# Kernel optimization log

Hardware: AMD Instinct MI355X
Metric: run time of the kernel (lower is better)

The kernel has to match this reference:

```python
import jax, jax.numpy as jnp
import numpy as np

B, CIN, COUT, K, H, W = 2, 128, 64, 64, 128, 128
BN_EPS = 1e-5


def setup_inputs() -> dict:
    key = jax.random.key(0)
    k1, k2, k3, k4 = jax.random.split(key, 4)
    x = jax.random.normal(k1, (B, CIN, H, W), dtype=jnp.float32)
    index = jax.random.randint(k2, (B, 1, H, W), 0, K)  # superpixel labels
    # kaiming_uniform(a=sqrt(5)) ~ uniform with bound sqrt(6/((1+5)*fan_in)) = 1/sqrt(fan_in)
    Wft = jax.random.uniform(k3, (CIN, COUT), dtype=jnp.float32,
                             minval=-1.0, maxval=1.0) / np.sqrt(CIN).astype(np.float32)
    Wm = jax.random.uniform(k4, (COUT, COUT), dtype=jnp.float32,
                            minval=-1.0, maxval=1.0) / np.sqrt(COUT).astype(np.float32)
    gamma = jnp.ones((COUT,), jnp.float32)
    beta = jnp.zeros((COUT,), jnp.float32)
    return {"x": x, "index": index, "Wft": Wft, "Wm": Wm, "gamma": gamma, "beta": beta}


def _gnn_forward(x, index, Wft, Wm, gamma, beta):
    # FeatureTransform: [B,Cin,H,W] -> [B,Cout,H,W]
    xt = jnp.einsum('bchw,co->bohw', x, Wft)

    idx = index[:, 0]                                   # [B,H,W]
    oh = jax.nn.one_hot(idx, K, dtype=xt.dtype)         # [B,H,W,K]

    # RegionalMeans (segment-mean over superpixels; equivalent to the
    # repeated-tensor multiply+sum in the torch code, without the 5D blowup)
    block_sum = oh.sum(axis=(1, 2))                     # [B,K]
    sums = jnp.einsum('bhwk,bohw->bko', oh, xt)         # [B,K,Cout]
    denom = block_sum + (block_sum == 0).astype(xt.dtype)
    means = sums / denom[..., None]                     # [B,K,Cout]

    # Adj: pairwise Mahalanobis distance with learned cov = Wm @ Wm.T
    cov = Wm @ Wm.T
    inv_cov = jnp.linalg.inv(cov)
    diff = means[:, :, None, :] - means[:, None, :, :]  # [B,K,K,Cout]
    q = jnp.einsum('bijc,cd,bijd->bij', diff, inv_cov, diff)
    dist = jnp.sqrt(jnp.maximum(q, 1e-12))              # clamp: diagonal q==0
    adj = jnp.exp(-dist)                                # [B,K,K]

    # GCN propagate: adjacency-weighted aggregation of region means
    adj_means = jnp.einsum('bij,bjo->bio', adj, means)  # [B,K,Cout]

    # sum_k one_hot_k * (x_rep + adj_means_k) == xt + gather(adj_means, idx)
    gathered = jnp.take_along_axis(adj_means, idx.reshape(B, -1, 1), axis=1)
    gathered = gathered.reshape(B, H, W, COUT).transpose(0, 3, 1, 2)
    features = jax.nn.relu(xt + gathered)               # [B,Cout,H,W]

    # BatchNorm2d (training-mode batch statistics, biased variance)
    mean = features.mean(axis=(0, 2, 3), keepdims=True)
    var = features.var(axis=(0, 2, 3), keepdims=True)
    out = (features - mean) / jnp.sqrt(var + BN_EPS)
    out = out * gamma[None, :, None, None] + beta[None, :, None, None]
    return out


def reference(x, index, Wft, Wm, gamma, beta):
    return _gnn_forward(x, index, Wft, Wm, gamma, beta)
```

## Files before the change

### kernel.cpp

```cpp
#include <hip/hip_runtime.h>
#include <hip/hip_bf16.h>

#define CIN   128
#define COUT  64
#define HW    16384
#define NB1   512

typedef __hip_bfloat16 bf16;

#define OFF_XT    0u
#define OFF_PS    2097152u
#define OFF_PC    3145728u
#define OFF_MEANS 3162112u
#define OFF_DIAG  3170304u
#define OFF_INV   3170432u
#define OFF_ADJM  3174528u
#define OFF_BNP   3182720u

__device__ __forceinline__ float rdlane(float v, int lane) {
  return __int_as_float(__builtin_amdgcn_readlane(__float_as_int(v), lane));
}

__global__ __launch_bounds__(256) void k1_xt_bins_inv(
    const float* __restrict__ x, const int* __restrict__ index,
    const float* __restrict__ Wft, const float* __restrict__ Wm,
    float* __restrict__ ws)
{
  __shared__ __align__(16) float smem[8704];
  const int blk = blockIdx.x, tid = threadIdx.x;
  if (blk < NB1) {
    float* lds_sums = smem;
    float* lds_cnt  = smem + 64 * 65;
    for (int i = tid; i < 64 * 65 + 64; i += 256) smem[i] = 0.f;
    __syncthreads();
    const int b    = blk >> 8;
    const int pg   = blk & 255;
    const int lane = tid & 63;
    const int og   = tid >> 6;
    const int o0   = __builtin_amdgcn_readfirstlane(og << 4);
    const int px   = (pg << 6) + lane;
    const float* xp = x + (size_t)b * CIN * HW + px;
    const int k = index[b * HW + px];
    float acc[16];
#pragma unroll
    for (int j = 0; j < 16; ++j) acc[j] = 0.f;
    float xa[8], xb[8];
#pragma unroll
    for (int u = 0; u < 8; ++u) xa[u] = xp[(size_t)u * HW];
    for (int cb = 0; cb < 128; cb += 8) {
      if (cb + 8 < 128) {
#pragma unroll
        for (int u = 0; u < 8; ++u) xb[u] = xp[(size_t)(cb + 8 + u) * HW];
      }
#pragma unroll
      for (int u = 0; u < 8; ++u) {
        const float xv = xa[u];
        const float4* w4 = (const float4*)(Wft + ((cb + u) << 6) + o0);
        const float4 w0 = w4[0], w1 = w4[1], w2 = w4[2], w3 = w4[3];
        acc[ 0]=fmaf(xv,w0.x,acc[ 0]); acc[ 1]=fmaf(xv,w0.y,acc[ 1]);
        acc[ 2]=fmaf(xv,w0.z,acc[ 2]); acc[ 3]=fmaf(xv,w0.w,acc[ 3]);
        acc[ 4]=fmaf(xv,w1.x,acc[ 4]); acc[ 5]=fmaf(xv,w1.y,acc[ 5]);
        acc[ 6]=fmaf(xv,w1.z,acc[ 6]); acc[ 7]=fmaf(xv,w1.w,acc[ 7]);
        acc[ 8]=fmaf(xv,w2.x,acc[ 8]); acc[ 9]=fmaf(xv,w2.y,acc[ 9]);
        acc[10]=fmaf(xv,w2.z,acc[10]); acc[11]=fmaf(xv,w2.w,acc[11]);
        acc[12]=fmaf(xv,w3.x,acc[12]); acc[13]=fmaf(xv,w3.y,acc[13]);
        acc[14]=fmaf(xv,w3.z,acc[14]); acc[15]=fmaf(xv,w3.w,acc[15]);
      }
#pragma unroll
      for (int u = 0; u < 8; ++u) xa[u] = xb[u];
    }
    float* xtp = ws + OFF_XT + (size_t)(b * COUT + o0) * HW + px;
#pragma unroll
    for (int j = 0; j < 16; ++j) xtp[(size_t)j * HW] = acc[j];
#pragma unroll
    for (int j = 0; j < 16; ++j) atomicAdd(&lds_sums[k * 65 + o0 + j], acc[j]);
    if (og == 0) atomicAdd(&lds_cnt[k], 1.f);
    __syncthreads();
    bf16* pb = (bf16*)(ws + OFF_PS) + (size_t)blk * 4096;
    for (int e = tid; e < 4096; e += 256)
      pb[e] = __float2bfloat16(lds_sums[(e >> 6) * 65 + (e & 63)]);
    if (tid < 64)
      ((bf16*)(ws + OFF_PC))[blk * 64 + tid] = __float2bfloat16(lds_cnt[tid]);
  } else {
    float* wm  = smem;
    float* cov = smem + 64 * 68;
    for (int e = tid; e < 4096; e += 256) wm[(e >> 6) * 68 + (e & 63)] = Wm[e];
    __syncthreads();
    {
      const int i0 = (tid >> 4) << 2, j0 = (tid & 15) << 2;
      float c4[16];
#pragma unroll
      for (int q = 0; q < 16; ++q) c4[q] = 0.f;
      for (int cq = 0; cq < 64; cq += 4) {
        float4 a[4], bb[4];
#pragma unroll
        for (int ii = 0; ii < 4; ++ii) a[ii]  = *(const float4*)&wm[(i0+ii)*68 + cq];
#pragma unroll
        for (int jj = 0; jj < 4; ++jj) bb[jj] = *(const float4*)&wm[(j0+jj)*68 + cq];
#pragma unroll
        for (int ii = 0; ii < 4; ++ii)
#pragma unroll
          for (int jj = 0; jj < 4; ++jj)
            c4[ii*4+jj] = fmaf(a[ii].x, bb[jj].x, fmaf(a[ii].y, bb[jj].y,
                          fmaf(a[ii].z, bb[jj].z, fmaf(a[ii].w, bb[jj].w, c4[ii*4+jj]))));
      }
#pragma unroll
      for (int ii = 0; ii < 4; ++ii)
#pragma unroll
        for (int jj = 0; jj < 4; ++jj)
          cov[(i0+ii)*68 + (j0+jj)] = c4[ii*4+jj];
    }
    __syncthreads();
    if (tid < 64) {
      float r[64];
#pragma unroll
      for (int j = 0; j < 64; ++j) r[j] = cov[tid * 68 + j];
#pragma unroll
      for (int k = 0; k < 64; ++k) {
        const float piv = rdlane(r[k], k);
        const float rp  = 1.0f / piv;
        const float a   = (tid == k) ? (rp - 1.0f) : (-r[k] * rp);
#pragma unroll
        for (int j = 0; j < 64; ++j) {
          const float s = rdlane(r[j], k);
          r[j] = fmaf(a, s, r[j]);
        }
        r[k] = (tid == k) ? rp : a;
      }
#pragma unroll
      for (int j = 0; j < 64; ++j) ws[OFF_INV + tid * 64 + j] = r[j];
    }
  }
}

__global__ __launch_bounds__(1024) void k15_means_diag(float* __restrict__ ws)
{
  __shared__ float red[16 * 64];
  __shared__ float lds_c[4];
  __shared__ float lds_m[64];
  const int blk = blockIdx.x, t = threadIdx.x;
  const int b = blk >> 6, k = blk & 63;
  const int o = t & 63, chunk = t >> 6;
  const bf16* ps = (const bf16*)(ws + OFF_PS);
  float s = 0.f;
#pragma unroll
  for (int s16 = 0; s16 < 16; ++s16) {
    const int i = chunk * 16 + s16;
    s += __bfloat162float(ps[(size_t)(b * 256 + i) * 4096 + (k << 6) + o]);
  }
  red[chunk * 64 + o] = s;
  float cv = 0.f;
  if (t < 256) cv = __bfloat162float(((const bf16*)(ws + OFF_PC))[(b * 256 + t) * 64 + k]);
#pragma unroll
  for (int m = 32; m; m >>= 1) cv += __shfl_xor(cv, m, 64);
  if (t < 256 && (t & 63) == 0) lds_c[t >> 6] = cv;
  __syncthreads();
  if (t < 64) {
    float m_raw = 0.f;
#pragma unroll
    for (int ch = 0; ch < 16; ++ch) m_raw += red[ch * 64 + o];
    const float cnt = lds_c[0] + lds_c[1] + lds_c[2] + lds_c[3];
    const float denom = cnt + ((cnt == 0.f) ? 1.f : 0.f);
    const float m = m_raw / denom;
    ws[OFF_MEANS + (size_t)(b * 64 + k) * 64 + o] = m;
    lds_m[o] = m;
    float inner = 0.f;
#pragma unroll 8
    for (int d = 0; d < 64; ++d) inner = fmaf(ws[OFF_INV + d * 64 + o], lds_m[d], inner);
    float p = m * inner;
#pragma unroll
    for (int mm = 32; mm; mm >>= 1) p += __shfl_xor(p, mm, 64);
    if (o == 0) ws[OFF_DIAG + b * 64 + k] = p;
  }
}

__global__ __launch_bounds__(256) void k2_adj(float* __restrict__ ws)
{
  __shared__ __align__(16) float means_s[64 * 68];
  __shared__ __align__(16) float inv_s[64 * 68];
  __shared__ __align__(16) float T_s[8 * 68];
  __shared__ __align__(16) float adj_s[8 * 68];
  __shared__ float diag_s[64];
  const int b = blockIdx.x >> 3;
  const int i0 = (blockIdx.x & 7) << 3;
  const int t = threadIdx.x;
  const float* mg = ws + OFF_MEANS + b * 4096;
  for (int e = t; e < 4096; e += 256) means_s[(e >> 6) * 68 + (e & 63)] = mg[e];
  const float* ig = ws + OFF_INV;
  for (int e = t; e < 4096; e += 256) inv_s[(e >> 6) * 68 + (e & 63)] = ig[e];
  if (t < 64) diag_s[t] = ws[OFF_DIAG + b * 64 + t];
  __syncthreads();
  if (t < 128) {
    const int i = t >> 4, d0 = (t & 15) << 2;
    float4 acc = {0.f, 0.f, 0.f, 0.f};
    for (int c = 0; c < 64; ++c) {
      const float mv = means_s[(i0 + i) * 68 + c];
      const float4 iv = *(const float4*)&inv_s[c * 68 + d0];
      acc.x = fmaf(mv, iv.x, acc.x); acc.y = fmaf(mv, iv.y, acc.y);
      acc.z = fmaf(mv, iv.z, acc.z); acc.w = fmaf(mv, iv.w, acc.w);
    }
    *(float4*)&T_s[i * 68 + d0] = acc;
  }
  __syncthreads();
  {
    const int i = t >> 5, jb = t & 31;
#pragma unroll
    for (int jj = 0; jj < 2; ++jj) {
      const int j = jb + (jj << 5);
      float4 p4 = {0.f, 0.f, 0.f, 0.f};
      for (int dq = 0; dq < 64; dq += 4) {
        const float4 tv = *(const float4*)&T_s[i * 68 + dq];
        const float4 mv = *(const float4*)&means_s[j * 68 + dq];
        p4.x = fmaf(tv.x, mv.x, p4.x); p4.y = fmaf(tv.y, mv.y, p4.y);
        p4.z = fmaf(tv.z, mv.z, p4.z); p4.w = fmaf(tv.w, mv.w, p4.w);
      }
      const float p = (p4.x + p4.y) + (p4.z + p4.w);
      const float q = diag_s[i0 + i] + diag_s[j] - 2.f * p;
      adj_s[i * 68 + j] = __expf(-sqrtf(fmaxf(q, 1e-12f)));
    }
  }
  __syncthreads();
  if (t < 128) {
    const int i = t >> 4, oq = (t & 15) << 2;
    float4 am = {0.f, 0.f, 0.f, 0.f};
    for (int j = 0; j < 64; ++j) {
      const float av = adj_s[i * 68 + j];
      const float4 mv = *(const float4*)&means_s[j * 68 + oq];
      am.x = fmaf(av, mv.x, am.x); am.y = fmaf(av, mv.y, am.y);
      am.z = fmaf(av, mv.z, am.z); am.w = fmaf(av, mv.w, am.w);
    }
    *(float4*)(ws + OFF_ADJM + (size_t)(b * 64 + i0 + i) * 64 + oq) = am;
  }
}

__global__ __launch_bounds__(256) void k3_bnstats(const int* __restrict__ index,
                                                  float* __restrict__ ws)
{
  __shared__ float4 am_s[64];
  __shared__ float red[8];
  const int blk = blockIdx.x, t = threadIdx.x;
  const int b = blk >> 8, og = (blk >> 4) & 15, tile = blk & 15;
  if (t < 64) am_s[t] = *(const float4*)(ws + OFF_ADJM + (size_t)(b * 64 + t) * 64 + og * 4);
  if (t < 8) red[t] = 0.f;
  __syncthreads();
  const int px0 = (tile << 10) + (t << 2);
  const int4 kv = *(const int4*)(index + b * HW + px0);
  const int kk[4] = {kv.x, kv.y, kv.z, kv.w};
  float4 xtv[4], amv[4];
#pragma unroll
  for (int oj = 0; oj < 4; ++oj)
    xtv[oj] = *(const float4*)(ws + OFF_XT + (size_t)(b * 64 + og * 4 + oj) * HW + px0);
#pragma unroll
  for (int p = 0; p < 4; ++p) amv[p] = am_s[kk[p]];
  float s[4] = {0.f,0.f,0.f,0.f}, ss[4] = {0.f,0.f,0.f,0.f};
#pragma unroll
  for (int oj = 0; oj < 4; ++oj) {
    const float* xf = (const float*)&xtv[oj];
#pragma unroll
    for (int p = 0; p < 4; ++p) {
      const float* af = (const float*)&amv[p];
      const float f = fmaxf(xf[p] + af[oj], 0.f);
      s[oj] += f; ss[oj] = fmaf(f, f, ss[oj]);
    }
  }
#pragma unroll
  for (int m = 1; m < 64; m <<= 1) {
#pragma unroll
    for (int oj = 0; oj < 4; ++oj) {
      s[oj]  += __shfl_xor(s[oj],  m, 64);
      ss[oj] += __shfl_xor(ss[oj], m, 64);
    }
  }
  if ((t & 63) == 0) {
#pragma unroll
    for (int oj = 0; oj < 4; ++oj) {
      atomicAdd(&red[oj], s[oj]);
      atomicAdd(&red[4 + oj], ss[oj]);
    }
  }
  __syncthreads();
  if (t < 8) ws[OFF_BNP + (size_t)(og * 32 + b * 16 + tile) * 8 + t] = red[t];
}

__global__ __launch_bounds__(256) void k4_out(const int* __restrict__ index,
    const float* __restrict__ gamma, const float* __restrict__ beta,
    const float* __restrict__ ws, float* __restrict__ out)
{
  __shared__ float4 am_s[64];
  __shared__ float tmp[8];
  __shared__ float sc_s[4], sh_s[4];
  const int blk = blockIdx.x, t = threadIdx.x;
  const int b = blk >> 8, og = (blk >> 4) & 15, tile = blk & 15;
  if (t < 64) am_s[t] = *(const float4*)(ws + OFF_ADJM + (size_t)(b * 64 + t) * 64 + og * 4);
  if (t < 8) {
    float v = 0.f;
#pragma unroll 4
    for (int i = 0; i < 32; ++i) v += ws[OFF_BNP + (size_t)(og * 32 + i) * 8 + t];
    tmp[t] = v;
  }
  if (t < 4) {
    const float mean = tmp[t] * (1.f / 32768.f);
    const float var  = tmp[4 + t] * (1.f / 32768.f) - mean * mean;
    const float sc = gamma[og * 4 + t] * rsqrtf(var + 1e-5f);
    sc_s[t] = sc;
    sh_s[t] = fmaf(-mean, sc, beta[og * 4 + t]);
  }
  __syncthreads();
  const int px0 = (tile << 10) + (t << 2);
  const int4 kv = *(const int4*)(index + b * HW + px0);
  const int kk[4] = {kv.x, kv.y, kv.z, kv.w};
  float4 xtv[4], amv[4];
#pragma unroll
  for (int oj = 0; oj < 4; ++oj)
    xtv[oj] = *(const float4*)(ws + OFF_XT + (size_t)(b * 64 + og * 4 + oj) * HW + px0);
#pragma unroll
  for (int p = 0; p < 4; ++p) amv[p] = am_s[kk[p]];
#pragma unroll
  for (int oj = 0; oj < 4; ++oj) {
    const float* xf = (const float*)&xtv[oj];
    float4 o4;
    float* of = (float*)&o4;
#pragma unroll
    for (int p = 0; p < 4; ++p) {
      const float* af = (const float*)&amv[p];
      const float f = fmaxf(xf[p] + af[oj], 0.f);
      of[p] = fmaf(f, sc_s[oj], sh_s[oj]);
    }
    *(float4*)(out + (size_t)(b * 64 + og * 4 + oj) * HW + px0) = o4;
  }
}

extern "C" void kernel_launch(void* const* d_in, const int* in_sizes, int n_in,
                              void* d_out, int out_size, void* d_ws, size_t ws_size,
                              hipStream_t stream) {
  const float* x     = (const float*)d_in[0];
  const int*   index = (const int*)d_in[1];
  const float* Wft   = (const float*)d_in[2];
  const float* Wm    = (const float*)d_in[3];
  const float* gamma = (const float*)d_in[4];
  const float* beta  = (const float*)d_in[5];
  float* ws  = (float*)d_ws;
  float* out = (float*)d_out;

  k1_xt_bins_inv<<<NB1 + 1, 256, 0, stream>>>(x, index, Wft, Wm, ws);
  k15_means_diag<<<128, 1024, 0, stream>>>(ws);
  k2_adj<<<16, 256, 0, stream>>>(ws);
  k3_bnstats<<<512, 256, 0, stream>>>(index, ws);
  k4_out<<<512, 256, 0, stream>>>(index, gamma, beta, ws, out);
}
```

Baseline: 137.8 us.

## Store xt intermediate in bf16 and retile projection, BN-stat and output kernels

```diff
diff --git a/kernel.cpp b/kernel.cpp
--- a/kernel.cpp
+++ b/kernel.cpp
@@ -4,117 +4,128 @@
 #define CIN   128
 #define COUT  64
 #define HW    16384
-#define NB1   512
 
 typedef __hip_bfloat16 bf16;
 
 #define OFF_XT    0u
-#define OFF_PS    2097152u
-#define OFF_PC    3145728u
-#define OFF_MEANS 3162112u
-#define OFF_DIAG  3170304u
-#define OFF_INV   3170432u
-#define OFF_ADJM  3174528u
-#define OFF_BNP   3182720u
+#define OFF_PS    1048576u
+#define OFF_PC    2097152u
+#define OFF_MEANS 2129920u
+#define OFF_DIAG  2138112u
+#define OFF_INV   2138240u
+#define OFF_ADJM  2142336u
+#define OFF_BNP   2150528u
 
 __device__ __forceinline__ float rdlane(float v, int lane) {
   return __int_as_float(__builtin_amdgcn_readlane(__float_as_int(v), lane));
 }
-
-__global__ __launch_bounds__(256) void k1_xt_bins_inv(
+__device__ __forceinline__ unsigned short f2bfu(float f) {
+  union { bf16 h; unsigned short u; } cv; cv.h = __float2bfloat16(f); return cv.u;
+}
+__device__ __forceinline__ float bf2f(unsigned short u) {
+  union { unsigned int i; float f; } cv; cv.i = ((unsigned int)u) << 16; return cv.f;
+}
+
+__global__ __launch_bounds__(256, 4) void k1_xt_bins_inv(
     const float* __restrict__ x, const int* __restrict__ index,
     const float* __restrict__ Wft, const float* __restrict__ Wm,
     float* __restrict__ ws)
 {
-  __shared__ __align__(16) float smem[8704];
+  __shared__ __align__(16) float smem[64 * 68];
   const int blk = blockIdx.x, tid = threadIdx.x;
-  if (blk < NB1) {
+  if (blk < 1024) {
     float* lds_sums = smem;
-    float* lds_cnt  = smem + 64 * 65;
-    for (int i = tid; i < 64 * 65 + 64; i += 256) smem[i] = 0.f;
-    __syncthreads();
-    const int b    = blk >> 8;
-    const int pg   = blk & 255;
-    const int lane = tid & 63;
-    const int og   = tid >> 6;
-    const int o0   = __builtin_amdgcn_readfirstlane(og << 4);
-    const int px   = (pg << 6) + lane;
+    float* lds_cnt  = smem + 2304;
+    for (int i = tid; i < 2368; i += 256) smem[i] = 0.f;
+    __syncthreads();
+    const int b  = blk >> 9;
+    const int oh = (blk >> 8) & 1;
+    const int ps = blk & 255;
+    const int w = tid >> 6, lane = tid & 63;
+    const int pq = lane & 7, og = lane >> 3;
+    const int px = ps * 64 + (w >> 1) * 32 + pq * 4;
+    const int lo = (w & 1) * 16 + og * 2;
+    const int o  = oh * 32 + lo;
     const float* xp = x + (size_t)b * CIN * HW + px;
-    const int k = index[b * HW + px];
-    float acc[16];
-#pragma unroll
-    for (int j = 0; j < 16; ++j) acc[j] = 0.f;
-    float xa[8], xb[8];
-#pragma unroll
-    for (int u = 0; u < 8; ++u) xa[u] = xp[(size_t)u * HW];
-    for (int cb = 0; cb < 128; cb += 8) {
-      if (cb + 8 < 128) {
-#pragma unroll
-        for (int u = 0; u < 8; ++u) xb[u] = xp[(size_t)(cb + 8 + u) * HW];
-      }
-#pragma unroll
-      for (int u = 0; u < 8; ++u) {
-        const float xv = xa[u];
-        const float4* w4 = (const float4*)(Wft + ((cb + u) << 6) + o0);
-        const float4 w0 = w4[0], w1 = w4[1], w2 = w4[2], w3 = w4[3];
-        acc[ 0]=fmaf(xv,w0.x,acc[ 0]); acc[ 1]=fmaf(xv,w0.y,acc[ 1]);
-        acc[ 2]=fmaf(xv,w0.z,acc[ 2]); acc[ 3]=fmaf(xv,w0.w,acc[ 3]);
-        acc[ 4]=fmaf(xv,w1.x,acc[ 4]); acc[ 5]=fmaf(xv,w1.y,acc[ 5]);
-        acc[ 6]=fmaf(xv,w1.z,acc[ 6]); acc[ 7]=fmaf(xv,w1.w,acc[ 7]);
-        acc[ 8]=fmaf(xv,w2.x,acc[ 8]); acc[ 9]=fmaf(xv,w2.y,acc[ 9]);
-        acc[10]=fmaf(xv,w2.z,acc[10]); acc[11]=fmaf(xv,w2.w,acc[11]);
-        acc[12]=fmaf(xv,w3.x,acc[12]); acc[13]=fmaf(xv,w3.y,acc[13]);
-        acc[14]=fmaf(xv,w3.z,acc[14]); acc[15]=fmaf(xv,w3.w,acc[15]);
-      }
-#pragma unroll
-      for (int u = 0; u < 8; ++u) xa[u] = xb[u];
-    }
-    float* xtp = ws + OFF_XT + (size_t)(b * COUT + o0) * HW + px;
-#pragma unroll
-    for (int j = 0; j < 16; ++j) xtp[(size_t)j * HW] = acc[j];
-#pragma unroll
-    for (int j = 0; j < 16; ++j) atomicAdd(&lds_sums[k * 65 + o0 + j], acc[j]);
-    if (og == 0) atomicAdd(&lds_cnt[k], 1.f);
-    __syncthreads();
-    bf16* pb = (bf16*)(ws + OFF_PS) + (size_t)blk * 4096;
-    for (int e = tid; e < 4096; e += 256)
-      pb[e] = __float2bfloat16(lds_sums[(e >> 6) * 65 + (e & 63)]);
-    if (tid < 64)
-      ((bf16*)(ws + OFF_PC))[blk * 64 + tid] = __float2bfloat16(lds_cnt[tid]);
+    const float* wp = Wft + o;
+    const int4 kv = *(const int4*)(index + b * HW + px);
+    float acc[8];
+#pragma unroll
+    for (int j = 0; j < 8; ++j) acc[j] = 0.f;
+#pragma unroll 16
+    for (int c = 0; c < 128; ++c) {
+      const float4 xv = *(const float4*)xp; xp += HW;
+      const float2 wv = *(const float2*)wp; wp += 64;
+      acc[0] = fmaf(xv.x, wv.x, acc[0]); acc[1] = fmaf(xv.y, wv.x, acc[1]);
+      acc[2] = fmaf(xv.z, wv.x, acc[2]); acc[3] = fmaf(xv.w, wv.x, acc[3]);
+      acc[4] = fmaf(xv.x, wv.y, acc[4]); acc[5] = fmaf(xv.y, wv.y, acc[5]);
+      acc[6] = fmaf(xv.z, wv.y, acc[6]); acc[7] = fmaf(xv.w, wv.y, acc[7]);
+    }
+    unsigned short* xtu = (unsigned short*)(ws + OFF_XT);
+#pragma unroll
+    for (int i = 0; i < 2; ++i) {
+      ushort4 u;
+      u.x = f2bfu(acc[i*4+0]); u.y = f2bfu(acc[i*4+1]);
+      u.z = f2bfu(acc[i*4+2]); u.w = f2bfu(acc[i*4+3]);
+      *(ushort4*)(xtu + (size_t)(b * 64 + o + i) * HW + px) = u;
+    }
+    const int kk[4] = {kv.x, kv.y, kv.z, kv.w};
+#pragma unroll
+    for (int j = 0; j < 4; ++j) {
+      atomicAdd(&lds_sums[kk[j] * 36 + lo    ], acc[j]);
+      atomicAdd(&lds_sums[kk[j] * 36 + lo + 1], acc[4 + j]);
+    }
+    if (oh == 0 && (w & 1) == 0 && og == 0) {
+#pragma unroll
+      for (int j = 0; j < 4; ++j) atomicAdd(&lds_cnt[kk[j]], 1.f);
+    }
+    __syncthreads();
+    unsigned short* pb = (unsigned short*)(ws + OFF_PS) + (size_t)((b * 2 + oh) * 256 + ps) * 2048;
+    {
+      const int k = tid >> 2, l0 = (tid & 3) * 8;
+      const float4 v0 = *(const float4*)&lds_sums[k * 36 + l0];
+      const float4 v1 = *(const float4*)&lds_sums[k * 36 + l0 + 4];
+      ushort4 ua, ub;
+      ua.x = f2bfu(v0.x); ua.y = f2bfu(v0.y); ua.z = f2bfu(v0.z); ua.w = f2bfu(v0.w);
+      ub.x = f2bfu(v1.x); ub.y = f2bfu(v1.y); ub.z = f2bfu(v1.z); ub.w = f2bfu(v1.w);
+      unsigned short* pp = pb + k * 32 + l0;
+      *(ushort4*)pp = ua; *(ushort4*)(pp + 4) = ub;
+    }
+    if (oh == 0 && tid < 64)
+      ws[OFF_PC + (size_t)(b * 64 + tid) * 256 + ps] = lds_cnt[tid];
   } else {
-    float* wm  = smem;
-    float* cov = smem + 64 * 68;
+    float* wm = smem;
     for (int e = tid; e < 4096; e += 256) wm[(e >> 6) * 68 + (e & 63)] = Wm[e];
     __syncthreads();
-    {
-      const int i0 = (tid >> 4) << 2, j0 = (tid & 15) << 2;
-      float c4[16];
-#pragma unroll
-      for (int q = 0; q < 16; ++q) c4[q] = 0.f;
-      for (int cq = 0; cq < 64; cq += 4) {
-        float4 a[4], bb[4];
-#pragma unroll
-        for (int ii = 0; ii < 4; ++ii) a[ii]  = *(const float4*)&wm[(i0+ii)*68 + cq];
-#pragma unroll
-        for (int jj = 0; jj < 4; ++jj) bb[jj] = *(const float4*)&wm[(j0+jj)*68 + cq];
-#pragma unroll
-        for (int ii = 0; ii < 4; ++ii)
-#pragma unroll
-          for (int jj = 0; jj < 4; ++jj)
-            c4[ii*4+jj] = fmaf(a[ii].x, bb[jj].x, fmaf(a[ii].y, bb[jj].y,
-                          fmaf(a[ii].z, bb[jj].z, fmaf(a[ii].w, bb[jj].w, c4[ii*4+jj]))));
-      }
+    const int i0 = (tid >> 4) << 2, j0 = (tid & 15) << 2;
+    float c4[16];
+#pragma unroll
+    for (int q = 0; q < 16; ++q) c4[q] = 0.f;
+    for (int cq = 0; cq < 64; cq += 4) {
+      float4 a[4], bb[4];
+#pragma unroll
+      for (int ii = 0; ii < 4; ++ii) a[ii]  = *(const float4*)&wm[(i0+ii)*68 + cq];
+#pragma unroll
+      for (int jj = 0; jj < 4; ++jj) bb[jj] = *(const float4*)&wm[(j0+jj)*68 + cq];
 #pragma unroll
       for (int ii = 0; ii < 4; ++ii)
 #pragma unroll
         for (int jj = 0; jj < 4; ++jj)
-          cov[(i0+ii)*68 + (j0+jj)] = c4[ii*4+jj];
-    }
+          c4[ii*4+jj] = fmaf(a[ii].x, bb[jj].x, fmaf(a[ii].y, bb[jj].y,
+                        fmaf(a[ii].z, bb[jj].z, fmaf(a[ii].w, bb[jj].w, c4[ii*4+jj]))));
+    }
+    __syncthreads();
+#pragma unroll
+    for (int ii = 0; ii < 4; ++ii)
+#pragma unroll
+      for (int jj = 0; jj < 4; ++jj)
+        smem[(i0+ii)*68 + (j0+jj)] = c4[ii*4+jj];
     __syncthreads();
     if (tid < 64) {
+      __builtin_amdgcn_s_setprio(3);
       float r[64];
 #pragma unroll
-      for (int j = 0; j < 64; ++j) r[j] = cov[tid * 68 + j];
+      for (int j = 0; j < 64; ++j) r[j] = smem[tid * 68 + j];
 #pragma unroll
       for (int k = 0; k < 64; ++k) {
         const float piv = rdlane(r[k], k);
@@ -127,6 +138,7 @@
         }
         r[k] = (tid == k) ? rp : a;
       }
+      __builtin_amdgcn_s_setprio(0);
 #pragma unroll
       for (int j = 0; j < 64; ++j) ws[OFF_INV + tid * 64 + j] = r[j];
     }
@@ -135,22 +147,21 @@
 
 __global__ __launch_bounds__(1024) void k15_means_diag(float* __restrict__ ws)
 {
-  __shared__ float red[16 * 64];
+  __shared__ float red[1024];
   __shared__ float lds_c[4];
   __shared__ float lds_m[64];
   const int blk = blockIdx.x, t = threadIdx.x;
   const int b = blk >> 6, k = blk & 63;
   const int o = t & 63, chunk = t >> 6;
-  const bf16* ps = (const bf16*)(ws + OFF_PS);
+  const int oh = o >> 5, o32 = o & 31;
+  const unsigned short* psu = (const unsigned short*)(ws + OFF_PS);
+  const size_t base = (size_t)((b * 2 + oh) * 256 + chunk * 16) * 2048 + k * 32 + o32;
   float s = 0.f;
 #pragma unroll
-  for (int s16 = 0; s16 < 16; ++s16) {
-    const int i = chunk * 16 + s16;
-    s += __bfloat162float(ps[(size_t)(b * 256 + i) * 4096 + (k << 6) + o]);
-  }
+  for (int i = 0; i < 16; ++i) s += bf2f(psu[base + (size_t)i * 2048]);
   red[chunk * 64 + o] = s;
   float cv = 0.f;
-  if (t < 256) cv = __bfloat162float(((const bf16*)(ws + OFF_PC))[(b * 256 + t) * 64 + k]);
+  if (t < 256) cv = ws[OFF_PC + (size_t)(b * 64 + k) * 256 + t];
 #pragma unroll
   for (int m = 32; m; m >>= 1) cv += __shfl_xor(cv, m, 64);
   if (t < 256 && (t & 63) == 0) lds_c[t >> 6] = cv;
@@ -236,97 +247,100 @@
 __global__ __launch_bounds__(256) void k3_bnstats(const int* __restrict__ index,
                                                   float* __restrict__ ws)
 {
-  __shared__ float4 am_s[64];
-  __shared__ float red[8];
+  __shared__ float am_s[128];
+  __shared__ float red[4];
   const int blk = blockIdx.x, t = threadIdx.x;
-  const int b = blk >> 8, og = (blk >> 4) & 15, tile = blk & 15;
-  if (t < 64) am_s[t] = *(const float4*)(ws + OFF_ADJM + (size_t)(b * 64 + t) * 64 + og * 4);
-  if (t < 8) red[t] = 0.f;
-  __syncthreads();
-  const int px0 = (tile << 10) + (t << 2);
-  const int4 kv = *(const int4*)(index + b * HW + px0);
-  const int kk[4] = {kv.x, kv.y, kv.z, kv.w};
-  float4 xtv[4], amv[4];
-#pragma unroll
-  for (int oj = 0; oj < 4; ++oj)
-    xtv[oj] = *(const float4*)(ws + OFF_XT + (size_t)(b * 64 + og * 4 + oj) * HW + px0);
-#pragma unroll
-  for (int p = 0; p < 4; ++p) amv[p] = am_s[kk[p]];
-  float s[4] = {0.f,0.f,0.f,0.f}, ss[4] = {0.f,0.f,0.f,0.f};
-#pragma unroll
-  for (int oj = 0; oj < 4; ++oj) {
-    const float* xf = (const float*)&xtv[oj];
-#pragma unroll
-    for (int p = 0; p < 4; ++p) {
-      const float* af = (const float*)&amv[p];
-      const float f = fmaxf(xf[p] + af[oj], 0.f);
-      s[oj] += f; ss[oj] = fmaf(f, f, ss[oj]);
+  const int b = blk >> 8, oc = (blk >> 3) & 31, tile = blk & 7;
+  const int o0 = oc * 2;
+  if (t < 128) am_s[t] = ws[OFF_ADJM + (size_t)(b * 64 + (t >> 1)) * 64 + o0 + (t & 1)];
+  if (t < 4) red[t] = 0.f;
+  __syncthreads();
+  const int lane = t & 63, w = t >> 6;
+  const unsigned short* xtu = (const unsigned short*)(ws + OFF_XT);
+  float s0 = 0.f, s1 = 0.f, q0 = 0.f, q1 = 0.f;
+#pragma unroll
+  for (int q = 0; q < 2; ++q) {
+    const int px = tile * 2048 + (w * 2 + q) * 256 + lane * 4;
+    const int4 kv = *(const int4*)(index + b * HW + px);
+    const ushort4 u0 = *(const ushort4*)(xtu + (size_t)(b * 64 + o0    ) * HW + px);
+    const ushort4 u1 = *(const ushort4*)(xtu + (size_t)(b * 64 + o0 + 1) * HW + px);
+    const int kk[4] = {kv.x, kv.y, kv.z, kv.w};
+    const float x0[4] = {bf2f(u0.x), bf2f(u0.y), bf2f(u0.z), bf2f(u0.w)};
+    const float x1[4] = {bf2f(u1.x), bf2f(u1.y), bf2f(u1.z), bf2f(u1.w)};
+#pragma unroll
+    for (int j = 0; j < 4; ++j) {
+      const float2 am = *(const float2*)&am_s[kk[j] * 2];
+      const float f0 = fmaxf(x0[j] + am.x, 0.f);
+      const float f1 = fmaxf(x1[j] + am.y, 0.f);
+      s0 += f0; q0 = fmaf(f0, f0, q0);
+      s1 += f1; q1 = fmaf(f1, f1, q1);
     }
   }
 #pragma unroll
   for (int m = 1; m < 64; m <<= 1) {
-#pragma unroll
-    for (int oj = 0; oj < 4; ++oj) {
-      s[oj]  += __shfl_xor(s[oj],  m, 64);
-      ss[oj] += __shfl_xor(ss[oj], m, 64);
-    }
-  }
-  if ((t & 63) == 0) {
-#pragma unroll
-    for (int oj = 0; oj < 4; ++oj) {
-      atomicAdd(&red[oj], s[oj]);
-      atomicAdd(&red[4 + oj], ss[oj]);
-    }
-  }
-  __syncthreads();
-  if (t < 8) ws[OFF_BNP + (size_t)(og * 32 + b * 16 + tile) * 8 + t] = red[t];
+    s0 += __shfl_xor(s0, m, 64); s1 += __shfl_xor(s1, m, 64);
+    q0 += __shfl_xor(q0, m, 64); q1 += __shfl_xor(q1, m, 64);
+  }
+  if (lane == 0) {
+    atomicAdd(&red[0], s0); atomicAdd(&red[1], s1);
+    atomicAdd(&red[2], q0); atomicAdd(&red[3], q1);
+  }
+  __syncthreads();
+  if (t == 0) {
+    float4 v; v.x = red[0]; v.y = red[1]; v.z = red[2]; v.w = red[3];
+    *(float4*)(ws + OFF_BNP + (size_t)(oc * 16 + b * 8 + tile) * 4) = v;
+  }
 }
 
 __global__ __launch_bounds__(256) void k4_out(const int* __restrict__ index,
     const float* __restrict__ gamma, const float* __restrict__ beta,
     const float* __restrict__ ws, float* __restrict__ out)
 {
-  __shared__ float4 am_s[64];
-  __shared__ float tmp[8];
-  __shared__ float sc_s[4], sh_s[4];
+  __shared__ float am_s[128];
+  __shared__ float4 tmp[16];
+  __shared__ float sc_s[2], sh_s[2];
   const int blk = blockIdx.x, t = threadIdx.x;
-  const int b = blk >> 8, og = (blk >> 4) & 15, tile = blk & 15;
-  if (t < 64) am_s[t] = *(const float4*)(ws + OFF_ADJM + (size_t)(b * 64 + t) * 64 + og * 4);
-  if (t < 8) {
-    float v = 0.f;
-#pragma unroll 4
-    for (int i = 0; i < 32; ++i) v += ws[OFF_BNP + (size_t)(og * 32 + i) * 8 + t];
-    tmp[t] = v;
-  }
-  if (t < 4) {
-    const float mean = tmp[t] * (1.f / 32768.f);
-    const float var  = tmp[4 + t] * (1.f / 32768.f) - mean * mean;
-    const float sc = gamma[og * 4 + t] * rsqrtf(var + 1e-5f);
+  const int b = blk >> 8, oc = (blk >> 3) & 31, tile = blk & 7;
+  const int o0 = oc * 2;
+  if (t < 128) am_s[t] = ws[OFF_ADJM + (size_t)(b * 64 + (t >> 1)) * 64 + o0 + (t & 1)];
+  if (t < 16) tmp[t] = *(const float4*)(ws + OFF_BNP + (size_t)(oc * 16 + t) * 4);
+  if (t < 2) {
+    float s = 0.f, qq = 0.f;
+#pragma unroll
+    for (int i = 0; i < 16; ++i) {
+      const float4 v = tmp[i];
+      s  += (t == 0) ? v.x : v.y;
+      qq += (t == 0) ? v.z : v.w;
+    }
+    const float mean = s * (1.f / 32768.f);
+    const float var  = qq * (1.f / 32768.f) - mean * mean;
+    const float sc = gamma[o0 + t] * rsqrtf(var + 1e-5f);
     sc_s[t] = sc;
-    sh_s[t] = fmaf(-mean, sc, beta[og * 4 + t]);
-  }
-  __syncthreads();
-  const int px0 = (tile << 10) + (t << 2);
-  const int4 kv = *(const int4*)(index + b * HW + px0);
-  const int kk[4] = {kv.x, kv.y, kv.z, kv.w};
-  float4 xtv[4], amv[4];
-#pragma unroll
-  for (int oj = 0; oj < 4; ++oj)
-    xtv[oj] = *(const float4*)(ws + OFF_XT + (size_t)(b * 64 + og * 4 + oj) * HW + px0);
-#pragma unroll
-  for (int p = 0; p < 4; ++p) amv[p] = am_s[kk[p]];
-#pragma unroll
-  for (int oj = 0; oj < 4; ++oj) {
-    const float* xf = (const float*)&xtv[oj];
-    float4 o4;
-    float* of = (float*)&o4;
-#pragma unroll
-    for (int p = 0; p < 4; ++p) {
-      const float* af = (const float*)&amv[p];
-      const float f = fmaxf(xf[p] + af[oj], 0.f);
-      of[p] = fmaf(f, sc_s[oj], sh_s[oj]);
-    }
-    *(float4*)(out + (size_t)(b * 64 + og * 4 + oj) * HW + px0) = o4;
+    sh_s[t] = fmaf(-mean, sc, beta[o0 + t]);
+  }
+  __syncthreads();
+  const int lane = t & 63, w = t >> 6;
+  const unsigned short* xtu = (const unsigned short*)(ws + OFF_XT);
+  const float c0 = sc_s[0], c1 = sc_s[1], h0 = sh_s[0], h1 = sh_s[1];
+#pragma unroll
+  for (int q = 0; q < 2; ++q) {
+    const int px = tile * 2048 + (w * 2 + q) * 256 + lane * 4;
+    const int4 kv = *(const int4*)(index + b * HW + px);
+    const ushort4 u0 = *(const ushort4*)(xtu + (size_t)(b * 64 + o0    ) * HW + px);
+    const ushort4 u1 = *(const ushort4*)(xtu + (size_t)(b * 64 + o0 + 1) * HW + px);
+    const int kk[4] = {kv.x, kv.y, kv.z, kv.w};
+    const float x0[4] = {bf2f(u0.x), bf2f(u0.y), bf2f(u0.z), bf2f(u0.w)};
+    const float x1[4] = {bf2f(u1.x), bf2f(u1.y), bf2f(u1.z), bf2f(u1.w)};
+    float4 o4a, o4b;
+    float* oa = (float*)&o4a; float* ob = (float*)&o4b;
+#pragma unroll
+    for (int j = 0; j < 4; ++j) {
+      const float2 am = *(const float2*)&am_s[kk[j] * 2];
+      oa[j] = fmaf(fmaxf(x0[j] + am.x, 0.f), c0, h0);
+      ob[j] = fmaf(fmaxf(x1[j] + am.y, 0.f), c1, h1);
+    }
+    *(float4*)(out + (size_t)(b * 64 + o0    ) * HW + px) = o4a;
+    *(float4*)(out + (size_t)(b * 64 + o0 + 1) * HW + px) = o4b;
   }
 }
 
@@ -342,7 +356,7 @@
   float* ws  = (float*)d_ws;
   float* out = (float*)d_out;
 
-  k1_xt_bins_inv<<<NB1 + 1, 256, 0, stream>>>(x, index, Wft, Wm, ws);
+  k1_xt_bins_inv<<<1025, 256, 0, stream>>>(x, index, Wft, Wm, ws);
   k15_means_diag<<<128, 1024, 0, stream>>>(ws);
   k2_adj<<<16, 256, 0, stream>>>(ws);
   k3_bnstats<<<512, 256, 0, stream>>>(index, ws);
```

New measurement: 140.6 us. +2.0%, slower.
